# Kernel optimization log

Hardware: AMD Instinct MI355X
Metric: run time of the kernel (lower is better)

Reference implementation:

```python
import jax, jax.numpy as jnp
import numpy as np

B, N, F_IN, H = 32, 1024, 64, 24


def setup_inputs() -> dict:
    key = jax.random.key(0)
    k1, k2 = jax.random.split(key)
    xt = jax.random.normal(k1, (B, N, F_IN), dtype=jnp.float32)
    # nn.Linear init scale ~ 1/sqrt(in_feats)
    W = jax.random.normal(k2, (F_IN, H), dtype=jnp.float32) / jnp.sqrt(jnp.float32(F_IN))
    b = jnp.zeros((H,), dtype=jnp.float32)
    return {"xt": xt, "W": W, "b": b}


def reference(xt, W, b):
    # Z = relu(Linear(xt)) : (B, N, H)
    Z = jax.nn.relu(jnp.einsum("bnf,fh->bnh", xt, W) + b)
    # raw similarity adjacency (B, N, N)
    A = jnp.einsum("bnh,bmh->bnm", Z, Z)
    # symmetric softmax
    A = 0.5 * (jax.nn.softmax(A, axis=-1) + jax.nn.softmax(A, axis=-2))
    # self loops
    A = A + jnp.eye(N, dtype=A.dtype)[None, :, :]
    # Kipf normalization D^-1/2 A D^-1/2 (diag bmm == row/col broadcast scale)
    degree = jnp.clip(jnp.sum(A, axis=-1), 1e-6, None)  # (B, N)
    d_inv_sqrt = degree ** -0.5
    A_normalized = A * d_inv_sqrt[:, :, None] * d_inv_sqrt[:, None, :]
    return A_normalized
```

## Files before the change

### kernel.cpp

```cpp
#include <hip/hip_runtime.h>

#define BB 32
#define NN 1024
#define FIN 64
#define HH 24
#define SQRT_LOG2E 1.2011224087864498f

typedef __attribute__((ext_vector_type(8))) short short8;
typedef __attribute__((ext_vector_type(4))) float floatx4;

static __device__ inline unsigned short bf16_rtne(float f) {
    unsigned u = __float_as_uint(f);
    unsigned r = u + 0x7FFFu + ((u >> 16) & 1u);
    return (unsigned short)(r >> 16);
}

__global__ void k_z(const float* __restrict__ xt, const float* __restrict__ W,
                    const float* __restrict__ bias, unsigned short* __restrict__ Zhl) {
    __shared__ float Wl[FIN * HH];
    int t = threadIdx.x;
    for (int i = t; i < FIN * HH; i += 256) Wl[i] = W[i];
    __syncthreads();

    int row = blockIdx.x * 256 + t;

    const float* xr = xt + (size_t)row * FIN;
    float x[FIN];
    #pragma unroll
    for (int k4 = 0; k4 < FIN / 4; ++k4) {
        float4 v = reinterpret_cast<const float4*>(xr)[k4];
        x[4 * k4 + 0] = v.x; x[4 * k4 + 1] = v.y;
        x[4 * k4 + 2] = v.z; x[4 * k4 + 3] = v.w;
    }

    unsigned short u[64];
    #pragma unroll
    for (int i = 0; i < 64; ++i) u[i] = 0;

    #pragma unroll
    for (int hg = 0; hg < HH / 4; ++hg) {
        float4 acc = reinterpret_cast<const float4*>(bias)[hg];
        #pragma unroll
        for (int k = 0; k < FIN; ++k) {
            float4 w = *reinterpret_cast<const float4*>(&Wl[k * HH + hg * 4]);
            acc.x += x[k] * w.x; acc.y += x[k] * w.y;
            acc.z += x[k] * w.z; acc.w += x[k] * w.w;
        }
        float zs[4] = { fmaxf(acc.x, 0.f) * SQRT_LOG2E, fmaxf(acc.y, 0.f) * SQRT_LOG2E,
                        fmaxf(acc.z, 0.f) * SQRT_LOG2E, fmaxf(acc.w, 0.f) * SQRT_LOG2E };
        #pragma unroll
        for (int j = 0; j < 4; ++j) {
            int h = hg * 4 + j;
            unsigned short hb = bf16_rtne(zs[j]);
            float hf = __uint_as_float((unsigned)hb << 16);
            u[h] = hb;
            u[32 + h] = bf16_rtne(zs[j] - hf);
        }
    }

    unsigned short* dst = Zhl + ((size_t)row << 6);
    #pragma unroll
    for (int i = 0; i < 8; ++i)
        reinterpret_cast<uint4*>(dst)[i] = *reinterpret_cast<const uint4*>(&u[i * 8]);
}


#define STAGE_CHUNK(m0)                                                                  \
    for (int i = t; i < 1024; i += 256) {                                                \
        int row_ = i >> 3, c_ = i & 7;                                                   \
        uint4 v_ = *reinterpret_cast<const uint4*>(                                      \
            Zhl + (((size_t)b * NN + (m0) + row_) << 6) + (c_ << 3));                    \
        *reinterpret_cast<uint4*>(&Bs[(((c_ << 7) + (row_ ^ c_)) << 3)]) = v_;           \
    }

#define LOAD_N_FRAGS()                                                                   \
    const unsigned short* nrow_ = Zhl + (((size_t)b * NN + n0w + r15) << 6) + (g << 3);  \
    short8 nh = *reinterpret_cast<const short8*>(nrow_);                                 \
    short8 nl = *reinterpret_cast<const short8*>(nrow_ + 32);

#define MFMA_TILE(mt)                                                                    \
    int roff = (mt) * 16 + r15;                                                          \
    short8 mh = *reinterpret_cast<const short8*>(&Bs[((g << 7) + (roff ^ g)) << 3]);     \
    short8 ml = *reinterpret_cast<const short8*>(                                        \
        &Bs[(((g + 4) << 7) + (roff ^ (g + 4))) << 3]);                                  \
    floatx4 acc = {0.f, 0.f, 0.f, 0.f};                                                  \
    acc = __builtin_amdgcn_mfma_f32_16x16x32_bf16(mh, nh, acc, 0, 0, 0);                 \
    acc = __builtin_amdgcn_mfma_f32_16x16x32_bf16(mh, nl, acc, 0, 0, 0);                 \
    acc = __builtin_amdgcn_mfma_f32_16x16x32_bf16(ml, nh, acc, 0, 0, 0);

__global__ __launch_bounds__(256) void k_rowsum(
        const unsigned short* __restrict__ Zhl, float* __restrict__ ps) {
    __shared__ unsigned short Bs[128 * 64];
    int t = threadIdx.x, lane = t & 63;
    int r15 = lane & 15, g = lane >> 4;
    int b = blockIdx.z;
    int n0w = blockIdx.x * 64 + (t >> 6) * 16;
    int mbase = blockIdx.y * 256;

    LOAD_N_FRAGS();

    float s = 0.f;

    #pragma unroll
    for (int ch = 0; ch < 2; ++ch) {
        __syncthreads();
        STAGE_CHUNK(mbase + ch * 128);
        __syncthreads();
        #pragma unroll
        for (int mt = 0; mt < 8; ++mt) {
            MFMA_TILE(mt);
            s += __builtin_amdgcn_exp2f(acc[0]) + __builtin_amdgcn_exp2f(acc[1])
               + __builtin_amdgcn_exp2f(acc[2]) + __builtin_amdgcn_exp2f(acc[3]);
        }
    }

    s += __shfl_xor(s, 16, 64);
    s += __shfl_xor(s, 32, 64);
    if (g == 0)
        ps[((size_t)blockIdx.y * BB + b) * NN + n0w + r15] = s;
}

__global__ __launch_bounds__(256) void k_colsum(
        const unsigned short* __restrict__ Zhl, const float* __restrict__ ps,
        float* __restrict__ pc) {
    __shared__ unsigned short Bs[128 * 64];
    __shared__ float rmS[256];
    int t = threadIdx.x, lane = t & 63;
    int r15 = lane & 15, g = lane >> 4;
    int b = blockIdx.z;
    int n0w = blockIdx.x * 64 + (t >> 6) * 16;
    int mbase = blockIdx.y * 256;

    {
        size_t o = (size_t)b * NN + mbase + t;
        float sm = ps[o] + ps[32768 + o] + ps[65536 + o] + ps[98304 + o];
        rmS[t] = 1.0f / sm;
    }

    LOAD_N_FRAGS();

    float c = 0.f;

    #pragma unroll
    for (int ch = 0; ch < 2; ++ch) {
        __syncthreads();
        STAGE_CHUNK(mbase + ch * 128);
        __syncthreads();
        #pragma unroll
        for (int mt = 0; mt < 8; ++mt) {
            MFMA_TILE(mt);
            float4 rm4 = *reinterpret_cast<const float4*>(&rmS[ch * 128 + mt * 16 + g * 4]);
            c += __builtin_amdgcn_exp2f(acc[0]) * rm4.x + __builtin_amdgcn_exp2f(acc[1]) * rm4.y
               + __builtin_amdgcn_exp2f(acc[2]) * rm4.z + __builtin_amdgcn_exp2f(acc[3]) * rm4.w;
        }
    }

    c += __shfl_xor(c, 16, 64);
    c += __shfl_xor(c, 32, 64);
    if (g == 0)
        pc[((size_t)blockIdx.y * BB + b) * NN + n0w + r15] = c;
}

__global__ __launch_bounds__(256) void k_out(
        const unsigned short* __restrict__ Zhl, const float* __restrict__ ps,
        const float* __restrict__ pc, float* __restrict__ out) {
    __shared__ unsigned short Bs[128 * 64];
    __shared__ float emS[256], dvmS[256];
    int t = threadIdx.x, lane = t & 63;
    int r15 = lane & 15, g = lane >> 4;
    int b = blockIdx.z;
    int n0w = blockIdx.x * 64 + (t >> 6) * 16;
    int mbase = blockIdx.y * 256;

    {
        size_t o = (size_t)b * NN + mbase + t;
        float sm = ps[o] + ps[32768 + o] + ps[65536 + o] + ps[98304 + o];
        float cm = pc[o] + pc[32768 + o] + pc[65536 + o] + pc[98304 + o];
        emS[t]  = 0.5f / sm;
        dvmS[t] = rsqrtf(1.5f + 0.5f * cm);
    }

    int n = n0w + r15;
    float en, dvn;
    {
        size_t o = (size_t)b * NN + n;
        float sn = ps[o] + ps[32768 + o] + ps[65536 + o] + ps[98304 + o];
        float cn = pc[o] + pc[32768 + o] + pc[65536 + o] + pc[98304 + o];
        en  = 0.5f / sn;
        dvn = rsqrtf(1.5f + 0.5f * cn);
    }

    LOAD_N_FRAGS();

    float* orow = out + ((size_t)b * NN + n) * NN;

    #pragma unroll
    for (int ch = 0; ch < 2; ++ch) {
        int m0 = mbase + ch * 128;
        __syncthreads();
        STAGE_CHUNK(m0);
        __syncthreads();
        #pragma unroll
        for (int mt = 0; mt < 8; ++mt) {
            MFMA_TILE(mt);
            int mq = ch * 128 + mt * 16 + g * 4;
            float4 em4 = *reinterpret_cast<const float4*>(&emS[mq]);
            float4 dv4 = *reinterpret_cast<const float4*>(&dvmS[mq]);
            int mg = mbase + mq;
            float4 o;
            float w0 = dvn * dv4.x, w1 = dvn * dv4.y, w2 = dvn * dv4.z, w3 = dvn * dv4.w;
            o.x = __builtin_amdgcn_exp2f(acc[0]) * (en + em4.x) * w0;
            o.y = __builtin_amdgcn_exp2f(acc[1]) * (en + em4.y) * w1;
            o.z = __builtin_amdgcn_exp2f(acc[2]) * (en + em4.z) * w2;
            o.w = __builtin_amdgcn_exp2f(acc[3]) * (en + em4.w) * w3;
            if (n == mg + 0) o.x += w0;
            if (n == mg + 1) o.y += w1;
            if (n == mg + 2) o.z += w2;
            if (n == mg + 3) o.w += w3;
            *reinterpret_cast<float4*>(orow + mg) = o;
        }
    }
}

extern "C" void kernel_launch(void* const* d_in, const int* in_sizes, int n_in,
                              void* d_out, int out_size, void* d_ws, size_t ws_size,
                              hipStream_t stream) {
    const float* xt   = (const float*)d_in[0];
    const float* W    = (const float*)d_in[1];
    const float* bias = (const float*)d_in[2];
    float* out = (float*)d_out;
    float* ws  = (float*)d_ws;

    unsigned short* Zhl = (unsigned short*)ws;
    float* ps = ws + 1048576;
    float* pc = ws + 1048576 + 131072;

    k_z<<<dim3(BB * NN / 256), dim3(256), 0, stream>>>(xt, W, bias, Zhl);
    k_rowsum<<<dim3(16, 4, BB), dim3(256), 0, stream>>>(Zhl, ps);
    k_colsum<<<dim3(16, 4, BB), dim3(256), 0, stream>>>(Zhl, ps, pc);
    k_out<<<dim3(16, 4, BB), dim3(256), 0, stream>>>(Zhl, ps, pc, out);
}
```

Measured before the change: 83.10 us.

## Drop LDS staging of Z tiles and precompute row/col normalizers in tiny kernels

The three N×N passes no longer stage 128-row chunks of Z into shared memory behind barriers. Each wave now loads its MFMA operand fragments straight from global memory (served mostly by L1/L2), with a partially unrolled loop. The per-block reductions of the partial row and column sums move into two small kernels that write reciprocal and rsqrt vectors, which later kernels read directly. This removes syncthreads and LDS traffic but adds two kernel launches and more global/L1 load traffic per tile.

```diff
diff --git a/kernel.cpp b/kernel.cpp
--- a/kernel.cpp
+++ b/kernel.cpp
@@ -65,32 +65,23 @@
 }
 
 
-#define STAGE_CHUNK(m0)                                                                  \
-    for (int i = t; i < 1024; i += 256) {                                                \
-        int row_ = i >> 3, c_ = i & 7;                                                   \
-        uint4 v_ = *reinterpret_cast<const uint4*>(                                      \
-            Zhl + (((size_t)b * NN + (m0) + row_) << 6) + (c_ << 3));                    \
-        *reinterpret_cast<uint4*>(&Bs[(((c_ << 7) + (row_ ^ c_)) << 3)]) = v_;           \
-    }
-
 #define LOAD_N_FRAGS()                                                                   \
     const unsigned short* nrow_ = Zhl + (((size_t)b * NN + n0w + r15) << 6) + (g << 3);  \
     short8 nh = *reinterpret_cast<const short8*>(nrow_);                                 \
     short8 nl = *reinterpret_cast<const short8*>(nrow_ + 32);
 
-#define MFMA_TILE(mt)                                                                    \
-    int roff = (mt) * 16 + r15;                                                          \
-    short8 mh = *reinterpret_cast<const short8*>(&Bs[((g << 7) + (roff ^ g)) << 3]);     \
-    short8 ml = *reinterpret_cast<const short8*>(                                        \
-        &Bs[(((g + 4) << 7) + (roff ^ (g + 4))) << 3]);                                  \
-    floatx4 acc = {0.f, 0.f, 0.f, 0.f};                                                  \
+#define MFMA_TILE_G(tt)                                                                  \
+    const unsigned short* ap_ =                                                          \
+        Zhl + (((size_t)b * NN + mbase + (tt) * 16 + r15) << 6) + (g << 3);              \
+    short8 mh = *reinterpret_cast<const short8*>(ap_);                                   \
+    short8 ml = *reinterpret_cast<const short8*>(ap_ + 32);                              \
+    floatx4 acc = {0.f, 0.f, 0.f, 0.f};                                                 \
     acc = __builtin_amdgcn_mfma_f32_16x16x32_bf16(mh, nh, acc, 0, 0, 0);                 \
     acc = __builtin_amdgcn_mfma_f32_16x16x32_bf16(mh, nl, acc, 0, 0, 0);                 \
     acc = __builtin_amdgcn_mfma_f32_16x16x32_bf16(ml, nh, acc, 0, 0, 0);
 
 __global__ __launch_bounds__(256) void k_rowsum(
         const unsigned short* __restrict__ Zhl, float* __restrict__ ps) {
-    __shared__ unsigned short Bs[128 * 64];
     int t = threadIdx.x, lane = t & 63;
     int r15 = lane & 15, g = lane >> 4;
     int b = blockIdx.z;
@@ -100,18 +91,11 @@
     LOAD_N_FRAGS();
 
     float s = 0.f;
-
-    #pragma unroll
-    for (int ch = 0; ch < 2; ++ch) {
-        __syncthreads();
-        STAGE_CHUNK(mbase + ch * 128);
-        __syncthreads();
-        #pragma unroll
-        for (int mt = 0; mt < 8; ++mt) {
-            MFMA_TILE(mt);
-            s += __builtin_amdgcn_exp2f(acc[0]) + __builtin_amdgcn_exp2f(acc[1])
-               + __builtin_amdgcn_exp2f(acc[2]) + __builtin_amdgcn_exp2f(acc[3]);
-        }
+    #pragma unroll 4
+    for (int tt = 0; tt < 16; ++tt) {
+        MFMA_TILE_G(tt);
+        s += __builtin_amdgcn_exp2f(acc[0]) + __builtin_amdgcn_exp2f(acc[1])
+           + __builtin_amdgcn_exp2f(acc[2]) + __builtin_amdgcn_exp2f(acc[3]);
     }
 
     s += __shfl_xor(s, 16, 64);
@@ -120,39 +104,30 @@
         ps[((size_t)blockIdx.y * BB + b) * NN + n0w + r15] = s;
 }
 
+__global__ void k_sfin(const float* __restrict__ ps, float* __restrict__ rinv) {
+    int i = blockIdx.x * 256 + threadIdx.x;
+    rinv[i] = 1.0f / (ps[i] + ps[32768 + i] + ps[65536 + i] + ps[98304 + i]);
+}
+
 __global__ __launch_bounds__(256) void k_colsum(
-        const unsigned short* __restrict__ Zhl, const float* __restrict__ ps,
+        const unsigned short* __restrict__ Zhl, const float* __restrict__ rinv,
         float* __restrict__ pc) {
-    __shared__ unsigned short Bs[128 * 64];
-    __shared__ float rmS[256];
     int t = threadIdx.x, lane = t & 63;
     int r15 = lane & 15, g = lane >> 4;
     int b = blockIdx.z;
     int n0w = blockIdx.x * 64 + (t >> 6) * 16;
     int mbase = blockIdx.y * 256;
 
-    {
-        size_t o = (size_t)b * NN + mbase + t;
-        float sm = ps[o] + ps[32768 + o] + ps[65536 + o] + ps[98304 + o];
-        rmS[t] = 1.0f / sm;
-    }
-
     LOAD_N_FRAGS();
 
     float c = 0.f;
-
-    #pragma unroll
-    for (int ch = 0; ch < 2; ++ch) {
-        __syncthreads();
-        STAGE_CHUNK(mbase + ch * 128);
-        __syncthreads();
-        #pragma unroll
-        for (int mt = 0; mt < 8; ++mt) {
-            MFMA_TILE(mt);
-            float4 rm4 = *reinterpret_cast<const float4*>(&rmS[ch * 128 + mt * 16 + g * 4]);
-            c += __builtin_amdgcn_exp2f(acc[0]) * rm4.x + __builtin_amdgcn_exp2f(acc[1]) * rm4.y
-               + __builtin_amdgcn_exp2f(acc[2]) * rm4.z + __builtin_amdgcn_exp2f(acc[3]) * rm4.w;
-        }
+    #pragma unroll 4
+    for (int tt = 0; tt < 16; ++tt) {
+        MFMA_TILE_G(tt);
+        float4 rm4 = *reinterpret_cast<const float4*>(
+            &rinv[(size_t)b * NN + mbase + tt * 16 + g * 4]);
+        c += __builtin_amdgcn_exp2f(acc[0]) * rm4.x + __builtin_amdgcn_exp2f(acc[1]) * rm4.y
+           + __builtin_amdgcn_exp2f(acc[2]) * rm4.z + __builtin_amdgcn_exp2f(acc[3]) * rm4.w;
     }
 
     c += __shfl_xor(c, 16, 64);
@@ -161,64 +136,45 @@
         pc[((size_t)blockIdx.y * BB + b) * NN + n0w + r15] = c;
 }
 
+__global__ void k_cfin(const float* __restrict__ pc, float* __restrict__ dinv) {
+    int i = blockIdx.x * 256 + threadIdx.x;
+    dinv[i] = rsqrtf(1.5f + 0.5f * (pc[i] + pc[32768 + i] + pc[65536 + i] + pc[98304 + i]));
+}
+
 __global__ __launch_bounds__(256) void k_out(
-        const unsigned short* __restrict__ Zhl, const float* __restrict__ ps,
-        const float* __restrict__ pc, float* __restrict__ out) {
-    __shared__ unsigned short Bs[128 * 64];
-    __shared__ float emS[256], dvmS[256];
+        const unsigned short* __restrict__ Zhl, const float* __restrict__ rinv,
+        const float* __restrict__ dinv, float* __restrict__ out) {
     int t = threadIdx.x, lane = t & 63;
     int r15 = lane & 15, g = lane >> 4;
     int b = blockIdx.z;
     int n0w = blockIdx.x * 64 + (t >> 6) * 16;
     int mbase = blockIdx.y * 256;
 
-    {
-        size_t o = (size_t)b * NN + mbase + t;
-        float sm = ps[o] + ps[32768 + o] + ps[65536 + o] + ps[98304 + o];
-        float cm = pc[o] + pc[32768 + o] + pc[65536 + o] + pc[98304 + o];
-        emS[t]  = 0.5f / sm;
-        dvmS[t] = rsqrtf(1.5f + 0.5f * cm);
-    }
-
     int n = n0w + r15;
-    float en, dvn;
-    {
-        size_t o = (size_t)b * NN + n;
-        float sn = ps[o] + ps[32768 + o] + ps[65536 + o] + ps[98304 + o];
-        float cn = pc[o] + pc[32768 + o] + pc[65536 + o] + pc[98304 + o];
-        en  = 0.5f / sn;
-        dvn = rsqrtf(1.5f + 0.5f * cn);
-    }
+    float en  = 0.5f * rinv[(size_t)b * NN + n];
+    float dvn = dinv[(size_t)b * NN + n];
 
     LOAD_N_FRAGS();
 
     float* orow = out + ((size_t)b * NN + n) * NN;
 
-    #pragma unroll
-    for (int ch = 0; ch < 2; ++ch) {
-        int m0 = mbase + ch * 128;
-        __syncthreads();
-        STAGE_CHUNK(m0);
-        __syncthreads();
-        #pragma unroll
-        for (int mt = 0; mt < 8; ++mt) {
-            MFMA_TILE(mt);
-            int mq = ch * 128 + mt * 16 + g * 4;
-            float4 em4 = *reinterpret_cast<const float4*>(&emS[mq]);
-            float4 dv4 = *reinterpret_cast<const float4*>(&dvmS[mq]);
-            int mg = mbase + mq;
-            float4 o;
-            float w0 = dvn * dv4.x, w1 = dvn * dv4.y, w2 = dvn * dv4.z, w3 = dvn * dv4.w;
-            o.x = __builtin_amdgcn_exp2f(acc[0]) * (en + em4.x) * w0;
-            o.y = __builtin_amdgcn_exp2f(acc[1]) * (en + em4.y) * w1;
-            o.z = __builtin_amdgcn_exp2f(acc[2]) * (en + em4.z) * w2;
-            o.w = __builtin_amdgcn_exp2f(acc[3]) * (en + em4.w) * w3;
-            if (n == mg + 0) o.x += w0;
-            if (n == mg + 1) o.y += w1;
-            if (n == mg + 2) o.z += w2;
-            if (n == mg + 3) o.w += w3;
-            *reinterpret_cast<float4*>(orow + mg) = o;
-        }
+    #pragma unroll 4
+    for (int tt = 0; tt < 16; ++tt) {
+        MFMA_TILE_G(tt);
+        int mg = mbase + tt * 16 + g * 4;
+        float4 rm4 = *reinterpret_cast<const float4*>(&rinv[(size_t)b * NN + mg]);
+        float4 dv4 = *reinterpret_cast<const float4*>(&dinv[(size_t)b * NN + mg]);
+        float4 o;
+        float w0 = dvn * dv4.x, w1 = dvn * dv4.y, w2 = dvn * dv4.z, w3 = dvn * dv4.w;
+        o.x = __builtin_amdgcn_exp2f(acc[0]) * (en + 0.5f * rm4.x) * w0;
+        o.y = __builtin_amdgcn_exp2f(acc[1]) * (en + 0.5f * rm4.y) * w1;
+        o.z = __builtin_amdgcn_exp2f(acc[2]) * (en + 0.5f * rm4.z) * w2;
+        o.w = __builtin_amdgcn_exp2f(acc[3]) * (en + 0.5f * rm4.w) * w3;
+        if (n == mg + 0) o.x += w0;
+        if (n == mg + 1) o.y += w1;
+        if (n == mg + 2) o.z += w2;
+        if (n == mg + 3) o.w += w3;
+        *reinterpret_cast<float4*>(orow + mg) = o;
     }
 }
 
@@ -232,11 +188,15 @@
     float* ws  = (float*)d_ws;
 
     unsigned short* Zhl = (unsigned short*)ws;
-    float* ps = ws + 1048576;
-    float* pc = ws + 1048576 + 131072;
+    float* ps   = ws + 1048576;
+    float* pc   = ws + 1048576 + 131072;
+    float* rinv = ws + 1048576 + 262144;
+    float* dinv = ws + 1048576 + 294912;
 
     k_z<<<dim3(BB * NN / 256), dim3(256), 0, stream>>>(xt, W, bias, Zhl);
     k_rowsum<<<dim3(16, 4, BB), dim3(256), 0, stream>>>(Zhl, ps);
-    k_colsum<<<dim3(16, 4, BB), dim3(256), 0, stream>>>(Zhl, ps, pc);
-    k_out<<<dim3(16, 4, BB), dim3(256), 0, stream>>>(Zhl, ps, pc, out);
-}
+    k_sfin<<<dim3(128), dim3(256), 0, stream>>>(ps, rinv);
+    k_colsum<<<dim3(16, 4, BB), dim3(256), 0, stream>>>(Zhl, rinv, pc);
+    k_cfin<<<dim3(128), dim3(256), 0, stream>>>(pc, dinv);
+    k_out<<<dim3(16, 4, BB), dim3(256), 0, stream>>>(Zhl, rinv, dinv, out);
+}
```

Result: slower. 144.6 us (+74.0%).
